# Kernel tuning notes

Hardware: AMD Instinct MI355X
Metric: run time of the kernel (lower is better)

The kernel has to match this reference:

```python
import jax, jax.numpy as jnp
import numpy as np

# Fixed geometry from the module's voxel_dict
VOXEL = np.array([0.32, 0.32, 6.0], dtype=np.float32)
PC_MIN = np.array([-74.88, -74.88, -2.0], dtype=np.float32)
PC_MAX = np.array([74.88, 74.88, 4.0], dtype=np.float32)
NX, NY, NZ = 468, 468, 1          # round((max-min)/voxel) per axis
CANVAS = NZ * NY * NX             # 219024 voxels (batch_size = 1)
OFFSET = VOXEL / 2.0 + PC_MIN     # x/y/z_offset from __init__


def setup_inputs() -> dict:
    key = jax.random.key(0)
    k1, k2, k3, k4 = jax.random.split(key, 4)
    N = 400000
    # points uniformly inside the point-cloud range (dynamic voxelization keeps all)
    xyz = jax.random.uniform(k1, (N, 3), dtype=jnp.float32) * (PC_MAX - PC_MIN) * 0.999 + PC_MIN
    extra = jax.random.normal(k2, (N, 2), dtype=jnp.float32)
    points = jnp.concatenate([xyz, extra], axis=1)          # [N, 5]
    W1 = jax.random.normal(k3, (11, 64), dtype=jnp.float32) * 0.05
    W2 = jax.random.normal(k4, (128, 64), dtype=jnp.float32) * 0.05
    return {"points": points, "W1": W1, "W2": W2}


def _flat_voxel_index(xyz):
    # dynamic voxelization: integer voxel coord per point, (z, y, x) ordering
    c = jnp.floor((xyz - PC_MIN) / VOXEL).astype(jnp.int32)
    cx = jnp.clip(c[:, 0], 0, NX - 1)
    cy = jnp.clip(c[:, 1], 0, NY - 1)
    cz = jnp.clip(c[:, 2], 0, NZ - 1)
    flat = cz * (NY * NX) + cy * NX + cx                    # canvas index as in map_voxel_center_to_point
    return flat, cx, cy, cz


def reference(points, W1, W2):
    xyz = points[:, :3]
    flat, cx, cy, cz = _flat_voxel_index(xyz)

    # DynamicScatter mean (cluster_scatter)
    cnt = jax.ops.segment_sum(jnp.ones((points.shape[0],), jnp.float32), flat, num_segments=CANVAS)
    vsum = jax.ops.segment_sum(points, flat, num_segments=CANVAS)
    vmean = vsum / jnp.maximum(cnt, 1.0)[:, None]           # [CANVAS, 5]
    pmean = vmean[flat]                                     # gather voxel mean to points

    f_cluster = xyz - pmean[:, :3]
    centers = jnp.stack([cx, cy, cz], axis=1).astype(jnp.float32) * VOXEL + OFFSET
    f_center = xyz - centers
    features = jnp.concatenate([points, f_cluster, f_center], axis=-1)   # [N, 11]

    occ = (cnt > 0)[:, None]

    # PFN layer 1: Linear(bias=False) + ReLU, then scatter-max to voxels
    pf1 = jax.nn.relu(features @ W1)                        # [N, 64]
    v1 = jax.ops.segment_max(pf1, flat, num_segments=CANVAS)
    v1 = jnp.where(occ, v1, 0.0)                            # zero empty voxels (replaces -inf)

    # gather voxel max back to points, concat, PFN layer 2
    feat2 = jnp.concatenate([pf1, v1[flat]], axis=1)        # [N, 128]
    pf2 = jax.nn.relu(feat2 @ W2)                           # [N, 64]
    v2 = jax.ops.segment_max(pf2, flat, num_segments=CANVAS)
    v2 = jnp.where(occ, v2, 0.0)                            # [CANVAS, 64] dense voxel features
    return v2
```

## Files before the change

### kernel.cpp

```cpp
#include <hip/hip_runtime.h>

#define NXc 468
#define NYc 468
#define CANVASc (468 * 468)
#define NPTS 400000
#define RUN 16
#define NRUNS (NPTS / RUN)

#define PCMIN_X (-74.88f)
#define PCMIN_Y (-74.88f)
#define VOX_X 0.32f
#define VOX_Y 0.32f
#define OFF_X (-74.72f)
#define OFF_Y (-74.72f)
#define OFF_Z (1.0f)

typedef __attribute__((ext_vector_type(8))) short v8s;
typedef __attribute__((ext_vector_type(4))) float v4f;

static_assert(sizeof(__bf16) == 2, "bf16 must be 2 bytes");

__device__ __forceinline__ int rli(int x, int p) {
    return __builtin_amdgcn_readlane(x, p);
}

__device__ __forceinline__ void split8(const float* f, v8s& h, v8s& l) {
    #pragma unroll
    for (int i = 0; i < 8; i += 2) {
        __bf16 h0 = (__bf16)f[i];
        __bf16 h1 = (__bf16)f[i + 1];
        h[i]     = __builtin_bit_cast(short, h0);
        h[i + 1] = __builtin_bit_cast(short, h1);
        float l0 = f[i]     - (float)h0;
        float l1 = f[i + 1] - (float)h1;
        l[i]     = __builtin_bit_cast(short, (__bf16)l0);
        l[i + 1] = __builtin_bit_cast(short, (__bf16)l1);
    }
}

__device__ __forceinline__ int voxel_cell(float x, float y, int& cx, int& cy) {
    cx = (int)floorf((x - PCMIN_X) / VOX_X);
    cy = (int)floorf((y - PCMIN_Y) / VOX_Y);
    cx = min(max(cx, 0), NXc - 1);
    cy = min(max(cy, 0), NYc - 1);
    return cy * NXc + cx;
}

__global__ __launch_bounds__(256) void k_stats(const float* __restrict__ pts,
                                               int* __restrict__ cnt) {
    int i = blockIdx.x * 256 + threadIdx.x;
    if (i >= NPTS) return;
    float x = pts[i * 5 + 0], y = pts[i * 5 + 1];
    int cx, cy;
    int fl = voxel_cell(x, y, cx, cy);
    atomicAdd(&cnt[fl], 1);
}

__global__ __launch_bounds__(256) void k_alloc(const int* __restrict__ cnt,
                                               int* __restrict__ cursor,
                                               int* __restrict__ gcur) {
    int v = blockIdx.x * 256 + threadIdx.x;
    int lane = threadIdx.x & 63;
    int c = (v < CANVASc) ? cnt[v] : 0;
    int scan = c;
    #pragma unroll
    for (int off = 1; off < 64; off <<= 1) {
        int t = __shfl_up(scan, off, 64);
        if (lane >= off) scan += t;
    }
    int total = __shfl(scan, 63, 64);
    int base = 0;
    if (lane == 0 && total > 0) base = atomicAdd(gcur, total);
    base = __shfl(base, 0, 64);
    if (v < CANVASc) cursor[v] = base + scan - c;
}

__device__ __forceinline__ void gather_pt(const float* __restrict__ pts, int pi,
                                          float4& A, float& e1) {
    const float* pp = pts + (size_t)pi * 5;
    __builtin_memcpy(&A, pp, 16);
    e1 = pp[4];
}

__global__ __launch_bounds__(256) void k_scatter(const float* __restrict__ pts,
                                                 int* __restrict__ cursor,
                                                 float4* __restrict__ pos4,
                                                 float* __restrict__ e1b) {
    int i = blockIdx.x * 256 + threadIdx.x;
    if (i >= NPTS) return;
    float4 A; float e1;
    gather_pt(pts, i, A, e1);
    int cx, cy;
    int fl = voxel_cell(A.x, A.y, cx, cy);
    int pos = atomicAdd(&cursor[fl], 1);
    pos4[pos] = A;
    e1b[pos] = e1;
}

__global__ __launch_bounds__(256) void kV(const int* __restrict__ cnt,
                                          const int* __restrict__ cursor,
                                          const float4* __restrict__ pos4,
                                          float4* __restrict__ vmean4) {
    int v = blockIdx.x * 256 + threadIdx.x;
    if (v >= CANVASc) return;
    int c = cnt[v];
    if (c == 0) return;
    int start = cursor[v] - c;
    float sx = 0.f, sy = 0.f, sz = 0.f;
    for (int i = 0; i < c; i++) {
        float4 p = pos4[start + i];
        sx += p.x; sy += p.y; sz += p.z;
    }
    float inv = 1.0f / (float)c;
    vmean4[v] = make_float4(sx * inv, sy * inv, sz * inv, 0.f);
}

__global__ __launch_bounds__(256) void kW(const float* __restrict__ W1,
                                          const float* __restrict__ W2,
                                          v8s* __restrict__ w1frag,
                                          v8s* __restrict__ w2frag) {
    int tid = blockIdx.x * 256 + threadIdx.x;
    if (tid < 1024) {
        int f = tid >> 6, lane = tid & 63;
        int t = f >> 2, c = f & 3;
        int q = lane >> 4, n = lane & 15;
        float v[8];
        #pragma unroll
        for (int i = 0; i < 8; i++) v[i] = W2[(c * 32 + q * 8 + i) * 64 + t * 16 + n];
        v8s h, l;
        split8(v, h, l);
        w2frag[(f * 2 + 0) * 64 + lane] = h;
        w2frag[(f * 2 + 1) * 64 + lane] = l;
    } else if (tid < 1280) {
        int f = (tid - 1024) >> 6, lane = (tid - 1024) & 63;
        int q = lane >> 4, n = lane & 15;
        float v[8];
        #pragma unroll
        for (int i = 0; i < 8; i++) {
            int k = q * 8 + i;
            v[i] = (k < 11) ? W1[k * 64 + f * 16 + n] : 0.f;
        }
        v8s h, l;
        split8(v, h, l);
        w1frag[(f * 2 + 0) * 64 + lane] = h;
        w1frag[(f * 2 + 1) * 64 + lane] = l;
    }
}

struct PtRegs {
    float4 A;
    float  e1, fcx, fcy, fcz;
    float  mx, my, mz;
    int    vx;
};
__device__ __forceinline__ PtRegs load_pt(const float4* __restrict__ pos4,
                                          const float* __restrict__ e1b,
                                          const float4* __restrict__ vmean4,
                                          int base, int j) {
    PtRegs r;
    r.A = make_float4(0.f, 0.f, 0.f, 0.f);
    r.e1 = r.fcx = r.fcy = r.fcz = r.mx = r.my = r.mz = 0.f;
    r.vx = -1;
    int idx = -1;
    if (j < RUN) idx = base + j;
    else if (j == 16) idx = (base + RUN < NPTS) ? base + RUN : -1;
    else if (j == 17) idx = base - 1;
    if (idx >= 0) {
        float4 A = pos4[idx];
        int cx, cy;
        int vv = voxel_cell(A.x, A.y, cx, cy);
        r.vx = vv;
        if (j < RUN) {
            r.A = A;
            r.e1 = e1b[idx];
            r.fcx = A.x - (cx * VOX_X + OFF_X);
            r.fcy = A.y - (cy * VOX_Y + OFF_Y);
            r.fcz = A.z - OFF_Z;
            float4 m = vmean4[vv];
            r.mx = m.x; r.my = m.y; r.mz = m.z;
        }
    }
    return r;
}

#define PSTR 68

__device__ __forceinline__ void phase1_mfma(float (*s_pf)[PSTR], const PtRegs& P,
                                            const v8s* __restrict__ w1frag, int j) {
    if (j < RUN) {
        float* row = s_pf[j];
        row[0] = P.A.x; row[1] = P.A.y; row[2] = P.A.z; row[3] = P.A.w; row[4] = P.e1;
        row[5] = P.A.x - P.mx; row[6] = P.A.y - P.my; row[7] = P.A.z - P.mz;
        row[8] = P.fcx; row[9] = P.fcy; row[10] = P.fcz;
        #pragma unroll
        for (int t = 11; t < 16; t++) row[t] = 0.f;
    }
    __builtin_amdgcn_wave_barrier();

    const int m = j & 15, q = j >> 4;
    v8s fh = {0,0,0,0,0,0,0,0}, fl_ = {0,0,0,0,0,0,0,0};
    if (q < 2) {
        float f8[8];
        #pragma unroll
        for (int i = 0; i < 8; i++) f8[i] = s_pf[m][q * 8 + i];
        split8(f8, fh, fl_);
    }
    v4f d[4];
    #pragma unroll
    for (int t = 0; t < 4; t++) {
        v8s bh = w1frag[(t * 2 + 0) * 64 + j];
        v8s bl = w1frag[(t * 2 + 1) * 64 + j];
        v4f acc = {0.f, 0.f, 0.f, 0.f};
        acc = __builtin_amdgcn_mfma_f32_16x16x32_bf16(fh,  bh, acc, 0, 0, 0);
        acc = __builtin_amdgcn_mfma_f32_16x16x32_bf16(fl_, bh, acc, 0, 0, 0);
        acc = __builtin_amdgcn_mfma_f32_16x16x32_bf16(fh,  bl, acc, 0, 0, 0);
        d[t] = acc;
    }
    __builtin_amdgcn_wave_barrier();
    #pragma unroll
    for (int t = 0; t < 4; t++)
        #pragma unroll
        for (int r = 0; r < 4; r++)
            s_pf[q * 4 + r][t * 16 + m] = fmaxf(d[t][r], 0.f);
    __builtin_amdgcn_wave_barrier();
}

__global__ __launch_bounds__(256) void kA(const float4* __restrict__ pos4,
                                          const float* __restrict__ e1b,
                                          const float4* __restrict__ vmean4,
                                          const v8s* __restrict__ w1frag,
                                          float* __restrict__ v1) {
    __shared__ float s_pf[4][RUN][PSTR];
    int wslot = threadIdx.x >> 6;
    int wave = blockIdx.x * 4 + wslot;
    int j = threadIdx.x & 63;
    int base = wave * RUN;

    PtRegs P = load_pt(pos4, e1b, vmean4, base, j);
    phase1_mfma(s_pf[wslot], P, w1frag, j);

    const int first = rli(P.vx, 0), last = rli(P.vx, RUN - 1);
    const bool firstExt = (rli(P.vx, 17) == first);
    const bool lastExt  = (rli(P.vx, 16) == last);
    int vprev = first;
    float smax = 0.f;
    for (int p = 0; p < RUN; p++) {
        int vp = rli(P.vx, p);
        if (vp != vprev) {
            size_t o = (size_t)vprev * 64 + j;
            bool ua = (vprev == first && firstExt) || (vprev == last && lastExt);
            if (ua) atomicMax((int*)v1 + o, __float_as_int(smax));
            else v1[o] = smax;
            vprev = vp; smax = 0.f;
        }
        smax = fmaxf(smax, s_pf[wslot][p][j]);
    }
    {
        size_t o = (size_t)vprev * 64 + j;
        bool ua = (vprev == first && firstExt) || (vprev == last && lastExt);
        if (ua) atomicMax((int*)v1 + o, __float_as_int(smax));
        else v1[o] = smax;
    }
}

__global__ __launch_bounds__(256) void kB(const float4* __restrict__ pos4,
                                          const float* __restrict__ e1b,
                                          const float4* __restrict__ vmean4,
                                          const v8s* __restrict__ w1frag,
                                          const v8s* __restrict__ w2frag,
                                          const float* __restrict__ v1,
                                          float* __restrict__ out) {
    __shared__ float s_pf[4][RUN][PSTR];
    int wslot = threadIdx.x >> 6;
    int wave = blockIdx.x * 4 + wslot;
    int j = threadIdx.x & 63;
    int base = wave * RUN;

    PtRegs P = load_pt(pos4, e1b, vmean4, base, j);
    phase1_mfma(s_pf[wslot], P, w1frag, j);

    const int m = j & 15, q = j >> 4;

    v8s ah[4], al[4];
    #pragma unroll
    for (int c = 0; c < 2; c++) {
        float f[8];
        #pragma unroll
        for (int i = 0; i < 8; i++) f[i] = s_pf[wslot][m][c * 32 + q * 8 + i];
        split8(f, ah[c], al[c]);
    }
    int vx_m = __builtin_amdgcn_ds_bpermute(m << 2, P.vx);
    {
        const float* vr = v1 + (size_t)vx_m * 64 + q * 8;
        #pragma unroll
        for (int c = 2; c < 4; c++) {
            float f[8];
            #pragma unroll
            for (int i = 0; i < 8; i++) f[i] = vr[(c - 2) * 32 + i];
            split8(f, ah[c], al[c]);
        }
    }
    __builtin_amdgcn_wave_barrier();

    #pragma unroll
    for (int t = 0; t < 4; t++) {
        v8s bh[4], bl[4];
        #pragma unroll
        for (int c = 0; c < 4; c++) {
            bh[c] = w2frag[((t * 4 + c) * 2 + 0) * 64 + j];
            bl[c] = w2frag[((t * 4 + c) * 2 + 1) * 64 + j];
        }
        v4f acc = {0.f, 0.f, 0.f, 0.f};
        #pragma unroll
        for (int c = 0; c < 4; c++) {
            acc = __builtin_amdgcn_mfma_f32_16x16x32_bf16(ah[c], bh[c], acc, 0, 0, 0);
            acc = __builtin_amdgcn_mfma_f32_16x16x32_bf16(al[c], bh[c], acc, 0, 0, 0);
            acc = __builtin_amdgcn_mfma_f32_16x16x32_bf16(ah[c], bl[c], acc, 0, 0, 0);
        }
        #pragma unroll
        for (int r = 0; r < 4; r++) s_pf[wslot][q * 4 + r][t * 16 + m] = acc[r];
    }
    __builtin_amdgcn_wave_barrier();

    const int first = rli(P.vx, 0), last = rli(P.vx, RUN - 1);
    const bool firstExt = (rli(P.vx, 17) == first);
    const bool lastExt  = (rli(P.vx, 16) == last);
    int vprev = first;
    float smax = -3.4e38f;
    for (int p = 0; p < RUN; p++) {
        int vp = rli(P.vx, p);
        if (vp != vprev) {
            float r = fmaxf(smax, 0.f);
            size_t o = (size_t)vprev * 64 + j;
            bool ua = (vprev == first && firstExt) || (vprev == last && lastExt);
            if (ua) atomicMax((int*)out + o, __float_as_int(r));
            else out[o] = r;
            vprev = vp; smax = -3.4e38f;
        }
        smax = fmaxf(smax, s_pf[wslot][p][j]);
    }
    {
        float r = fmaxf(smax, 0.f);
        size_t o = (size_t)vprev * 64 + j;
        bool ua = (vprev == first && firstExt) || (vprev == last && lastExt);
        if (ua) atomicMax((int*)out + o, __float_as_int(r));
        else out[o] = r;
    }
}

extern "C" void kernel_launch(void* const* d_in, const int* in_sizes, int n_in,
                              void* d_out, int out_size, void* d_ws, size_t ws_size,
                              hipStream_t stream) {
    const float* pts = (const float*)d_in[0];
    const float* W1  = (const float*)d_in[1];
    const float* W2  = (const float*)d_in[2];
    float* out = (float*)d_out;

    float4* vmean4 = (float4*)d_ws;
    float*  v1     = (float*)(vmean4 + CANVASc);
    float4* pos4   = (float4*)(v1 + (size_t)CANVASc * 64);
    float*  e1b    = (float*)(pos4 + NPTS);
    v8s*    w2frag = (v8s*)(e1b + NPTS);
    v8s*    w1frag = w2frag + 2048;
    int*    cnt    = (int*)(w1frag + 512);
    int*    gcur   = cnt + CANVASc;
    int*    cursor = gcur + 1;

    hipMemsetAsync(cnt, 0, (size_t)(CANVASc + 1) * 4, stream);
    hipMemsetAsync(d_out, 0, (size_t)out_size * sizeof(float), stream);

    int gpts = (NPTS + 255) / 256;
    int gvox = (CANVASc + 255) / 256;
    k_stats  <<<gpts, 256, 0, stream>>>(pts, cnt);
    k_alloc  <<<gvox, 256, 0, stream>>>(cnt, cursor, gcur);
    k_scatter<<<gpts, 256, 0, stream>>>(pts, cursor, pos4, e1b);
    kW       <<<5, 256, 0, stream>>>(W1, W2, w1frag, w2frag);
    kV       <<<gvox, 256, 0, stream>>>(cnt, cursor, pos4, vmean4);
    kA       <<<NRUNS / 4, 256, 0, stream>>>(pos4, e1b, vmean4, w1frag, v1);
    kB       <<<NRUNS / 4, 256, 0, stream>>>(pos4, e1b, vmean4, w1frag, w2frag, v1, out);
}
```

Baseline: 246.8 us.

## Replace full output memset with targeted zeroing and prefetch v1 rows in kB

Drops the full-canvas memset of the output (~56 MB) and instead zeroes only empty voxels in kV, plus a new seam kernel that zeroes out/v1 entries for voxels whose points straddle run boundaries (so atomic max accumulation starts from zero). It also hoists the v1 gather in kB ahead of the phase-1 MFMA to overlap global load latency with compute. This relies on the assumption that non-seam occupied voxels are fully written by kA/kB, which adds a launch and a correctness dependency on the run-write semantics.

```diff
diff --git a/kernel.cpp b/kernel.cpp
--- a/kernel.cpp
+++ b/kernel.cpp
@@ -100,11 +100,18 @@
 __global__ __launch_bounds__(256) void kV(const int* __restrict__ cnt,
                                           const int* __restrict__ cursor,
                                           const float4* __restrict__ pos4,
-                                          float4* __restrict__ vmean4) {
+                                          float4* __restrict__ vmean4,
+                                          float4* __restrict__ out4) {
     int v = blockIdx.x * 256 + threadIdx.x;
     if (v >= CANVASc) return;
     int c = cnt[v];
-    if (c == 0) return;
+    if (c == 0) {
+        float4 z = make_float4(0.f, 0.f, 0.f, 0.f);
+        float4* o = out4 + (size_t)v * 16;
+        #pragma unroll
+        for (int i = 0; i < 16; i++) o[i] = z;
+        return;
+    }
     int start = cursor[v] - c;
     float sx = 0.f, sy = 0.f, sz = 0.f;
     for (int i = 0; i < c; i++) {
@@ -113,6 +120,25 @@
     }
     float inv = 1.0f / (float)c;
     vmean4[v] = make_float4(sx * inv, sy * inv, sz * inv, 0.f);
+}
+
+__global__ __launch_bounds__(256) void k_seam(const float4* __restrict__ pos4,
+                                              float4* __restrict__ v14,
+                                              float4* __restrict__ out4) {
+    int w = blockIdx.x * 256 + threadIdx.x;
+    if (w == 0 || w >= NRUNS) return;
+    int b = w * RUN;
+    float4 Pa = pos4[b - 1];
+    float4 Pb = pos4[b];
+    int cx, cy;
+    int va = voxel_cell(Pa.x, Pa.y, cx, cy);
+    int vb = voxel_cell(Pb.x, Pb.y, cx, cy);
+    if (va != vb) return;
+    float4 z = make_float4(0.f, 0.f, 0.f, 0.f);
+    float4* o = out4 + (size_t)va * 16;
+    float4* q = v14 + (size_t)va * 16;
+    #pragma unroll
+    for (int i = 0; i < 16; i++) { o[i] = z; q[i] = z; }
 }
 
 __global__ __launch_bounds__(256) void kW(const float* __restrict__ W1,
@@ -277,9 +303,20 @@
     int base = wave * RUN;
 
     PtRegs P = load_pt(pos4, e1b, vmean4, base, j);
+
+    const int m = j & 15, q = j >> 4;
+
+    int vx_m = __builtin_amdgcn_ds_bpermute(m << 2, P.vx);
+    float vf[16];
+    {
+        const float* vr = v1 + (size_t)vx_m * 64 + q * 8;
+        #pragma unroll
+        for (int c = 0; c < 2; c++)
+            #pragma unroll
+            for (int i = 0; i < 8; i++) vf[c * 8 + i] = vr[c * 32 + i];
+    }
+
     phase1_mfma(s_pf[wslot], P, w1frag, j);
-
-    const int m = j & 15, q = j >> 4;
 
     v8s ah[4], al[4];
     #pragma unroll
@@ -289,17 +326,8 @@
         for (int i = 0; i < 8; i++) f[i] = s_pf[wslot][m][c * 32 + q * 8 + i];
         split8(f, ah[c], al[c]);
     }
-    int vx_m = __builtin_amdgcn_ds_bpermute(m << 2, P.vx);
-    {
-        const float* vr = v1 + (size_t)vx_m * 64 + q * 8;
-        #pragma unroll
-        for (int c = 2; c < 4; c++) {
-            float f[8];
-            #pragma unroll
-            for (int i = 0; i < 8; i++) f[i] = vr[(c - 2) * 32 + i];
-            split8(f, ah[c], al[c]);
-        }
-    }
+    split8(vf + 0, ah[2], al[2]);
+    split8(vf + 8, ah[3], al[3]);
     __builtin_amdgcn_wave_barrier();
 
     #pragma unroll
@@ -367,15 +395,16 @@
     int*    cursor = gcur + 1;
 
     hipMemsetAsync(cnt, 0, (size_t)(CANVASc + 1) * 4, stream);
-    hipMemsetAsync(d_out, 0, (size_t)out_size * sizeof(float), stream);
 
     int gpts = (NPTS + 255) / 256;
     int gvox = (CANVASc + 255) / 256;
+    int gseam = (NRUNS + 255) / 256;
     k_stats  <<<gpts, 256, 0, stream>>>(pts, cnt);
     k_alloc  <<<gvox, 256, 0, stream>>>(cnt, cursor, gcur);
     k_scatter<<<gpts, 256, 0, stream>>>(pts, cursor, pos4, e1b);
     kW       <<<5, 256, 0, stream>>>(W1, W2, w1frag, w2frag);
-    kV       <<<gvox, 256, 0, stream>>>(cnt, cursor, pos4, vmean4);
+    kV       <<<gvox, 256, 0, stream>>>(cnt, cursor, pos4, vmean4, (float4*)out);
+    k_seam   <<<gseam, 256, 0, stream>>>(pos4, (float4*)v1, (float4*)out);
     kA       <<<NRUNS / 4, 256, 0, stream>>>(pos4, e1b, vmean4, w1frag, v1);
     kB       <<<NRUNS / 4, 256, 0, stream>>>(pos4, e1b, vmean4, w1frag, w2frag, v1, out);
 }
```

Result: no change. 243.9 us (-1.2%).
